# Performance work log

Measured on AMD Instinct MI355X. Metric: run time of the kernel, lower is better.

## Reference

```python
import jax, jax.numpy as jnp
import numpy as np

def setup_inputs() -> dict:
    key = jax.random.key(0)
    ks = jax.random.split(key, 7)
    T, B, I, H = 512, 128, 512, 512
    s = 1.0 / np.sqrt(H)
    return {
        "input": jax.random.normal(ks[0], (T, B, I), dtype=jnp.float32),
        "h0": jax.random.normal(ks[1], (B, H), dtype=jnp.float32),
        "c0": jax.random.normal(ks[2], (B, H), dtype=jnp.float32),
        "W_ih": jax.random.normal(ks[3], (4 * H, I), dtype=jnp.float32) * s,
        "W_hh": jax.random.normal(ks[4], (4 * H, H), dtype=jnp.float32) * s,
        "b_ih": jax.random.normal(ks[5], (4 * H,), dtype=jnp.float32) * s,
        "b_hh": jax.random.normal(ks[6], (4 * H,), dtype=jnp.float32) * s,
    }

def reference(input, h0, c0, W_ih, W_hh, b_ih, b_hh):
    H = h0.shape[-1]
    # Precompute input contribution for all timesteps: [T, B, 4H]
    x_gates = jnp.einsum('tbi,gi->tbg', input, W_ih) + b_ih + b_hh

    def step(carry, xg):
        h, c = carry
        gates = xg + h @ W_hh.T  # [B, 4H]
        i, f, g, o = jnp.split(gates, 4, axis=-1)
        i = jax.nn.sigmoid(i)
        f = jax.nn.sigmoid(f)
        g = jnp.tanh(g)
        o = jax.nn.sigmoid(o)
        c = f * c + i * g
        h = o * jnp.tanh(c)
        return (h, c), h

    (hT, cT), outputs = jax.lax.scan(step, (h0, c0), x_gates)
    return outputs, (hT, cT)
```

## Files before the change

kernel.cpp:

```cpp
#include <hip/hip_runtime.h>
#include <hip/hip_bf16.h>

#define T_STEPS 512
#define BATCH   128
#define IN      512
#define HID     512
#define KTOT    1024
#define BT      16
#define JT      32
#define NBT     8
#define NJT     16
#define BH      (BATCH * HID)

typedef __attribute__((ext_vector_type(8))) short bf16x8;
typedef __attribute__((ext_vector_type(4))) float f32x4;
typedef __attribute__((ext_vector_type(4))) unsigned int u32x4;

static __device__ __forceinline__ unsigned short f2bf(float f) {
    unsigned u = __float_as_uint(f);
    unsigned r = (u + 0x7FFFu + ((u >> 16) & 1u)) >> 16;
    return (unsigned short)r;
}
static __device__ __forceinline__ ushort4 pack4(float4 v) {
    ushort4 b4;
    b4.x = f2bf(v.x); b4.y = f2bf(v.y); b4.z = f2bf(v.z); b4.w = f2bf(v.w);
    return b4;
}
static __device__ __forceinline__ float tanh_fast(float x) {
    return 1.f - 2.f * __builtin_amdgcn_rcpf(1.f + __expf(2.f * x));
}
static __device__ __forceinline__ bool vld4(u32x4 v, unsigned tgtw) {
    return ((v[0] & 0xFFFF0000u) == tgtw) & ((v[1] & 0xFFFF0000u) == tgtw) &
           ((v[2] & 0xFFFF0000u) == tgtw) & ((v[3] & 0xFFFF0000u) == tgtw);
}

__global__ void prep_kernel(const float* __restrict__ W_ih, const float* __restrict__ W_hh,
                            const float* __restrict__ b_ih, const float* __restrict__ b_hh,
                            unsigned short* __restrict__ Wc, float* __restrict__ bias) {
    int idx = blockIdx.x * blockDim.x + threadIdx.x;
    int row = idx >> 8;
    int kq  = idx & 255;
    const float* src = (kq < 128) ? (W_ih + (size_t)row * IN + kq * 4)
                                  : (W_hh + (size_t)row * HID + (kq - 128) * 4);
    float4 v = *(const float4*)src;
    *(ushort4*)(Wc + (size_t)row * KTOT + kq * 4) = pack4(v);
    if (idx < 4 * HID) bias[idx] = b_ih[idx] + b_hh[idx];
}

__global__ __launch_bounds__(512, 2) void lstm_kernel(
    const float* __restrict__ xin, const float* __restrict__ h0,
    const float* __restrict__ c0, const unsigned short* __restrict__ Wc,
    const float* __restrict__ bias, float* __restrict__ out,
    unsigned* __restrict__ hseq)
{
    const int tid  = threadIdx.x;
    const int bid  = blockIdx.x;
    const int bt   = bid & 7;
    const int jt   = bid >> 3;
    const int wv   = tid >> 6;
    const int lane = tid & 63;
    const int ln15 = lane & 15;
    const int khi  = lane >> 4;

    __shared__ __align__(16) unsigned char smem[49152];

    const int gown = ln15 & 3;
    const int jj   = ln15 >> 2;
    const int jcol = jt * JT + wv * 4 + jj;
    const int wrow_idx = gown * HID + jcol;

    bf16x8 wfrag[32];
    {
        const unsigned short* wrow = Wc + (size_t)wrow_idx * KTOT;
        #pragma unroll
        for (int kk = 0; kk < 32; ++kk)
            wfrag[kk] = *(const bf16x8*)(wrow + kk * 32 + khi * 8);
    }
    const float biasv = bias[wrow_idx];

    float creg[4];
    #pragma unroll
    for (int R = 0; R < 4; ++R)
        creg[R] = c0[(size_t)(bt * BT + khi * 4 + R) * HID + jcol];

    const unsigned swz = (unsigned)((ln15 & 7) << 4);
    const int xrow0 = tid >> 7;
    const int xcol4 = tid & 127;

    const int q     = wv * 4 + khi;
    const int prow  = q >> 1;
    const int qh    = q & 1;
    const unsigned rsw = (unsigned)((prow & 7) << 4);

    #pragma unroll
    for (int i = 0; i < 4; ++i) {
        int row = xrow0 + 4 * i;
        unsigned off = ((unsigned)(xcol4 * 8)) ^ ((unsigned)((row & 7) << 4));
        float4 vx = *(const float4*)(xin + (size_t)(bt * BT + row) * IN + xcol4 * 4);
        *(ushort4*)(smem + (size_t)row * 1024 + off) = pack4(vx);
        float4 vh = *(const float4*)(h0 + (size_t)(bt * BT + row) * HID + xcol4 * 4);
        *(ushort4*)(smem + 16384 + (size_t)row * 1024 + off) = pack4(vh);
    }
    float4 xr[4];
    #pragma unroll
    for (int i = 0; i < 4; ++i)
        xr[i] = *(const float4*)(xin + (size_t)1 * (BATCH * IN)
                                     + (size_t)(bt * BT + xrow0 + 4 * i) * IN + xcol4 * 4);
    __syncthreads();

    f32x4 acc_x0 = {biasv, biasv, biasv, biasv};
    f32x4 acc_x1 = {0.f, 0.f, 0.f, 0.f};
    {
        const unsigned char* xrow_p = smem + (size_t)ln15 * 1024;
        #pragma unroll
        for (int kk = 0; kk < 16; ++kk) {
            unsigned off = ((unsigned)(kk * 64 + khi * 16)) ^ swz;
            bf16x8 af = *(const bf16x8*)(xrow_p + off);
            if (kk & 1) acc_x1 = __builtin_amdgcn_mfma_f32_16x16x32_bf16(af, wfrag[kk], acc_x1, 0, 0, 0);
            else        acc_x0 = __builtin_amdgcn_mfma_f32_16x16x32_bf16(af, wfrag[kk], acc_x0, 0, 0, 0);
        }
    }
    __syncthreads();

    #pragma unroll 1
    for (int t = 0; t < T_STEPS; ++t) {
        const unsigned hbase = 16384u + (unsigned)(t & 1) * 16384u;
        f32x4 acc0 = acc_x0;
        f32x4 acc1 = acc_x1;
        const unsigned char* hrow_p = smem + hbase + (size_t)ln15 * 1024;
        #pragma unroll
        for (int kk = 16; kk < 32; ++kk) {
            unsigned off = ((unsigned)((kk - 16) * 64 + khi * 16)) ^ swz;
            bf16x8 af = *(const bf16x8*)(hrow_p + off);
            if (kk & 1) acc1 = __builtin_amdgcn_mfma_f32_16x16x32_bf16(af, wfrag[kk], acc1, 0, 0, 0);
            else        acc0 = __builtin_amdgcn_mfma_f32_16x16x32_bf16(af, wfrag[kk], acc0, 0, 0, 0);
        }
        f32x4 accs = acc0 + acc1;

        float hR[4];
        const int srcbase = lane & 0x3C;
        #pragma unroll
        for (int R = 0; R < 4; ++R) {
            float x = accs[R];
            bool isg = (gown == 2);
            float e = __expf(isg ? 2.f * x : -x);
            float r = __builtin_amdgcn_rcpf(1.f + e);
            float a = isg ? 1.f - 2.f * r : r;
            float vi = __shfl(a, srcbase + 0);
            float vf = __shfl(a, srcbase + 1);
            float vg = __shfl(a, srcbase + 2);
            float vo = __shfl(a, srcbase + 3);
            float c = vf * creg[R] + vi * vg;
            creg[R] = c;
            hR[R] = vo * tanh_fast(c);
        }

        if (t == T_STEPS - 1) {
            #pragma unroll
            for (int R = 0; R < 4; ++R) {
                if (gown == R) {
                    size_t o2 = (size_t)(bt * BT + khi * 4 + R) * HID + jcol;
                    out[(size_t)t * BH + o2] = hR[R];
                    size_t base = (size_t)T_STEPS * BH;
                    out[base + o2] = hR[R];
                    out[base + BH + o2] = creg[R];
                }
            }
        } else {
            #pragma unroll
            for (int R = 0; R < 4; ++R) {
                if (gown == R) {
                    unsigned w = ((unsigned)(t + 1) << 16) | (unsigned)f2bf(hR[R]);
                    unsigned* hp = hseq + (size_t)(t & 1) * BH
                                        + (size_t)(bt * BT + khi * 4 + R) * HID + jcol;
                    asm volatile("global_store_dword %0, %1, off sc0 sc1"
                                 :: "v"(hp), "v"(w) : "memory");
                }
            }
            #pragma unroll
            for (int R = 0; R < 4; ++R) {
                if (gown == R)
                    out[(size_t)t * BH + (size_t)(bt * BT + khi * 4 + R) * HID + jcol] = hR[R];
            }

            #pragma unroll
            for (int i = 0; i < 4; ++i) {
                int row = xrow0 + 4 * i;
                unsigned off = ((unsigned)(xcol4 * 8)) ^ ((unsigned)((row & 7) << 4));
                *(ushort4*)(smem + (size_t)row * 1024 + off) = pack4(xr[i]);
            }

            asm volatile("s_waitcnt lgkmcnt(0)" ::: "memory");
            __builtin_amdgcn_s_barrier();

            const unsigned* pp = hseq + (size_t)(t & 1) * BH
                                      + (size_t)(bt * BT + prow) * HID + qh * 256 + ln15 * 4;
            const unsigned tgtw = (unsigned)(t + 1) << 16;
            u32x4 hv0, hv1, hv2, hv3;
            asm volatile(
                "global_load_dwordx4 %0, %4, off offset:0 sc0 sc1\n\t"
                "global_load_dwordx4 %1, %4, off offset:256 sc0 sc1\n\t"
                "global_load_dwordx4 %2, %4, off offset:512 sc0 sc1\n\t"
                "global_load_dwordx4 %3, %4, off offset:768 sc0 sc1"
                : "=&v"(hv0), "=&v"(hv1), "=&v"(hv2), "=&v"(hv3)
                : "v"(pp) : "memory");

            {
                int tn = (t + 2) & (T_STEPS - 1);
                #pragma unroll
                for (int i = 0; i < 4; ++i)
                    xr[i] = *(const float4*)(xin + (size_t)tn * (BATCH * IN)
                                                 + (size_t)(bt * BT + xrow0 + 4 * i) * IN + xcol4 * 4);
            }

            acc_x0 = f32x4{biasv, biasv, biasv, biasv};
            acc_x1 = f32x4{0.f, 0.f, 0.f, 0.f};
            {
                const unsigned char* xrow_p = smem + (size_t)ln15 * 1024;
                #pragma unroll
                for (int kk = 0; kk < 16; ++kk) {
                    unsigned off = ((unsigned)(kk * 64 + khi * 16)) ^ swz;
                    bf16x8 af = *(const bf16x8*)(xrow_p + off);
                    if (kk & 1) acc_x1 = __builtin_amdgcn_mfma_f32_16x16x32_bf16(af, wfrag[kk], acc_x1, 0, 0, 0);
                    else        acc_x0 = __builtin_amdgcn_mfma_f32_16x16x32_bf16(af, wfrag[kk], acc_x0, 0, 0, 0);
                }
            }

            asm volatile("s_waitcnt vmcnt(4)" ::: "memory");
            __builtin_amdgcn_sched_barrier(0);
            for (;;) {
                bool ok = vld4(hv0, tgtw) & vld4(hv1, tgtw) & vld4(hv2, tgtw) & vld4(hv3, tgtw);
                if (__ballot(ok) == ~0ull) break;
                asm volatile(
                    "global_load_dwordx4 %0, %4, off offset:0 sc0 sc1\n\t"
                    "global_load_dwordx4 %1, %4, off offset:256 sc0 sc1\n\t"
                    "global_load_dwordx4 %2, %4, off offset:512 sc0 sc1\n\t"
                    "global_load_dwordx4 %3, %4, off offset:768 sc0 sc1\n\t"
                    "s_waitcnt vmcnt(0)"
                    : "=&v"(hv0), "=&v"(hv1), "=&v"(hv2), "=&v"(hv3)
                    : "v"(pp) : "memory");
                __builtin_amdgcn_sched_barrier(0);
            }

            {
                unsigned hnb = 16384u + (unsigned)((t + 1) & 1) * 16384u;
                unsigned wbase = hnb + (unsigned)prow * 1024u;
                const u32x4 hv[4] = {hv0, hv1, hv2, hv3};
                #pragma unroll
                for (int sq = 0; sq < 4; ++sq) {
                    uint2 pk;
                    pk.x = (hv[sq][0] & 0xFFFFu) | (hv[sq][1] << 16);
                    pk.y = (hv[sq][2] & 0xFFFFu) | (hv[sq][3] << 16);
                    unsigned off = ((unsigned)(qh * 512 + sq * 128 + ln15 * 8)) ^ rsw;
                    *(uint2*)(smem + wbase + off) = pk;
                }
            }

            asm volatile("s_waitcnt lgkmcnt(0)" ::: "memory");
            __builtin_amdgcn_s_barrier();
        }
    }
}

extern "C" void kernel_launch(void* const* d_in, const int* in_sizes, int n_in,
                              void* d_out, int out_size, void* d_ws, size_t ws_size,
                              hipStream_t stream) {
    const float* input = (const float*)d_in[0];
    const float* h0    = (const float*)d_in[1];
    const float* c0    = (const float*)d_in[2];
    const float* W_ih  = (const float*)d_in[3];
    const float* W_hh  = (const float*)d_in[4];
    const float* b_ih  = (const float*)d_in[5];
    const float* b_hh  = (const float*)d_in[6];
    float* out = (float*)d_out;

    char* ws = (char*)d_ws;
    unsigned* hseq = (unsigned*)ws;
    float*    bias = (float*)(ws + 512 * 1024);
    unsigned short* Wc = (unsigned short*)(ws + 512 * 1024 + 16 * 1024);

    hipMemsetAsync(hseq, 0, 2 * BH * sizeof(unsigned), stream);
    prep_kernel<<<2048, 256, 0, stream>>>(W_ih, W_hh, b_ih, b_hh, Wc, bias);
    lstm_kernel<<<NBT * NJT, 512, 0, stream>>>(input, h0, c0, Wc, bias, out, hseq);
}
```

Measured before the change: 1.917 ms.

## Process two batch tiles per block, halving grid, and use DPP quad broadcast

```diff
diff --git a/kernel.cpp b/kernel.cpp
--- a/kernel.cpp
+++ b/kernel.cpp
@@ -8,7 +8,6 @@
 #define KTOT    1024
 #define BT      16
 #define JT      32
-#define NBT     8
 #define NJT     16
 #define BH      (BATCH * HID)
 
@@ -32,6 +31,11 @@
 static __device__ __forceinline__ bool vld4(u32x4 v, unsigned tgtw) {
     return ((v[0] & 0xFFFF0000u) == tgtw) & ((v[1] & 0xFFFF0000u) == tgtw) &
            ((v[2] & 0xFFFF0000u) == tgtw) & ((v[3] & 0xFFFF0000u) == tgtw);
+}
+template<int I>
+static __device__ __forceinline__ float qbcast(float x) {
+    return __uint_as_float((unsigned)__builtin_amdgcn_update_dpp(
+        (int)__float_as_uint(x), (int)__float_as_uint(x), I * 0x55, 0xF, 0xF, false));
 }
 
 __global__ void prep_kernel(const float* __restrict__ W_ih, const float* __restrict__ W_hh,
@@ -55,14 +59,16 @@
 {
     const int tid  = threadIdx.x;
     const int bid  = blockIdx.x;
-    const int bt   = bid & 7;
-    const int jt   = bid >> 3;
+    const int gp   = bid & 3;
+    const int jt   = bid >> 2;
+    const int btA  = gp * 2;
+    const int btB  = gp * 2 + 1;
     const int wv   = tid >> 6;
     const int lane = tid & 63;
     const int ln15 = lane & 15;
     const int khi  = lane >> 4;
 
-    __shared__ __align__(16) unsigned char smem[49152];
+    __shared__ __align__(16) unsigned char smem[98304];
 
     const int gown = ln15 & 3;
     const int jj   = ln15 >> 2;
@@ -78,10 +84,12 @@
     }
     const float biasv = bias[wrow_idx];
 
-    float creg[4];
+    float cregA[4], cregB[4];
     #pragma unroll
-    for (int R = 0; R < 4; ++R)
-        creg[R] = c0[(size_t)(bt * BT + khi * 4 + R) * HID + jcol];
+    for (int R = 0; R < 4; ++R) {
+        cregA[R] = c0[(size_t)(btA * BT + khi * 4 + R) * HID + jcol];
+        cregB[R] = c0[(size_t)(btB * BT + khi * 4 + R) * HID + jcol];
+    }
 
     const unsigned swz = (unsigned)((ln15 & 7) << 4);
     const int xrow0 = tid >> 7;
@@ -96,163 +104,239 @@
     for (int i = 0; i < 4; ++i) {
         int row = xrow0 + 4 * i;
         unsigned off = ((unsigned)(xcol4 * 8)) ^ ((unsigned)((row & 7) << 4));
-        float4 vx = *(const float4*)(xin + (size_t)(bt * BT + row) * IN + xcol4 * 4);
-        *(ushort4*)(smem + (size_t)row * 1024 + off) = pack4(vx);
-        float4 vh = *(const float4*)(h0 + (size_t)(bt * BT + row) * HID + xcol4 * 4);
-        *(ushort4*)(smem + 16384 + (size_t)row * 1024 + off) = pack4(vh);
-    }
-    float4 xr[4];
+        float4 vA = *(const float4*)(xin + (size_t)(btA * BT + row) * IN + xcol4 * 4);
+        *(ushort4*)(smem + (size_t)row * 1024 + off) = pack4(vA);
+        float4 vB = *(const float4*)(xin + (size_t)(btB * BT + row) * IN + xcol4 * 4);
+        *(ushort4*)(smem + 16384 + (size_t)row * 1024 + off) = pack4(vB);
+        float4 hA = *(const float4*)(h0 + (size_t)(btA * BT + row) * HID + xcol4 * 4);
+        *(ushort4*)(smem + 32768 + (size_t)row * 1024 + off) = pack4(hA);
+        float4 hB = *(const float4*)(h0 + (size_t)(btB * BT + row) * HID + xcol4 * 4);
+        *(ushort4*)(smem + 65536 + (size_t)row * 1024 + off) = pack4(hB);
+    }
+    float4 xrA[4], xrB[4];
     #pragma unroll
-    for (int i = 0; i < 4; ++i)
-        xr[i] = *(const float4*)(xin + (size_t)1 * (BATCH * IN)
-                                     + (size_t)(bt * BT + xrow0 + 4 * i) * IN + xcol4 * 4);
+    for (int i = 0; i < 4; ++i) {
+        xrA[i] = *(const float4*)(xin + (size_t)1 * (BATCH * IN)
+                                      + (size_t)(btA * BT + xrow0 + 4 * i) * IN + xcol4 * 4);
+        xrB[i] = *(const float4*)(xin + (size_t)1 * (BATCH * IN)
+                                      + (size_t)(btB * BT + xrow0 + 4 * i) * IN + xcol4 * 4);
+    }
     __syncthreads();
 
-    f32x4 acc_x0 = {biasv, biasv, biasv, biasv};
-    f32x4 acc_x1 = {0.f, 0.f, 0.f, 0.f};
+    f32x4 acc_xA0 = {biasv, biasv, biasv, biasv}, acc_xA1 = {0.f, 0.f, 0.f, 0.f};
+    f32x4 acc_xB0 = {biasv, biasv, biasv, biasv}, acc_xB1 = {0.f, 0.f, 0.f, 0.f};
     {
-        const unsigned char* xrow_p = smem + (size_t)ln15 * 1024;
+        const unsigned char* xa = smem + (size_t)ln15 * 1024;
+        const unsigned char* xb = smem + 16384 + (size_t)ln15 * 1024;
         #pragma unroll
         for (int kk = 0; kk < 16; ++kk) {
             unsigned off = ((unsigned)(kk * 64 + khi * 16)) ^ swz;
-            bf16x8 af = *(const bf16x8*)(xrow_p + off);
-            if (kk & 1) acc_x1 = __builtin_amdgcn_mfma_f32_16x16x32_bf16(af, wfrag[kk], acc_x1, 0, 0, 0);
-            else        acc_x0 = __builtin_amdgcn_mfma_f32_16x16x32_bf16(af, wfrag[kk], acc_x0, 0, 0, 0);
+            bf16x8 afA = *(const bf16x8*)(xa + off);
+            bf16x8 afB = *(const bf16x8*)(xb + off);
+            if (kk & 1) { acc_xA1 = __builtin_amdgcn_mfma_f32_16x16x32_bf16(afA, wfrag[kk], acc_xA1, 0, 0, 0);
+                          acc_xB1 = __builtin_amdgcn_mfma_f32_16x16x32_bf16(afB, wfrag[kk], acc_xB1, 0, 0, 0); }
+            else        { acc_xA0 = __builtin_amdgcn_mfma_f32_16x16x32_bf16(afA, wfrag[kk], acc_xA0, 0, 0, 0);
+                          acc_xB0 = __builtin_amdgcn_mfma_f32_16x16x32_bf16(afB, wfrag[kk], acc_xB0, 0, 0, 0); }
         }
     }
     __syncthreads();
 
     #pragma unroll 1
     for (int t = 0; t < T_STEPS; ++t) {
-        const unsigned hbase = 16384u + (unsigned)(t & 1) * 16384u;
-        f32x4 acc0 = acc_x0;
-        f32x4 acc1 = acc_x1;
-        const unsigned char* hrow_p = smem + hbase + (size_t)ln15 * 1024;
-        #pragma unroll
-        for (int kk = 16; kk < 32; ++kk) {
-            unsigned off = ((unsigned)((kk - 16) * 64 + khi * 16)) ^ swz;
-            bf16x8 af = *(const bf16x8*)(hrow_p + off);
-            if (kk & 1) acc1 = __builtin_amdgcn_mfma_f32_16x16x32_bf16(af, wfrag[kk], acc1, 0, 0, 0);
-            else        acc0 = __builtin_amdgcn_mfma_f32_16x16x32_bf16(af, wfrag[kk], acc0, 0, 0, 0);
+        const unsigned hsA = 32768u + (unsigned)(t & 1) * 16384u;
+        const unsigned hsB = 65536u + (unsigned)(t & 1) * 16384u;
+        float hRA[4], hRB[4];
+
+        {
+            f32x4 a0 = acc_xA0, a1 = acc_xA1;
+            const unsigned char* hp = smem + hsA + (size_t)ln15 * 1024;
+            #pragma unroll
+            for (int kk = 16; kk < 32; ++kk) {
+                unsigned off = ((unsigned)((kk - 16) * 64 + khi * 16)) ^ swz;
+                bf16x8 af = *(const bf16x8*)(hp + off);
+                if (kk & 1) a1 = __builtin_amdgcn_mfma_f32_16x16x32_bf16(af, wfrag[kk], a1, 0, 0, 0);
+                else        a0 = __builtin_amdgcn_mfma_f32_16x16x32_bf16(af, wfrag[kk], a0, 0, 0, 0);
+            }
+            f32x4 accs = a0 + a1;
+            #pragma unroll
+            for (int R = 0; R < 4; ++R) {
+                float x = accs[R];
+                bool isg = (gown == 2);
+                float e = __expf(isg ? 2.f * x : -x);
+                float r = __builtin_amdgcn_rcpf(1.f + e);
+                float a = isg ? 1.f - 2.f * r : r;
+                float vi = qbcast<0>(a), vf = qbcast<1>(a), vg = qbcast<2>(a), vo = qbcast<3>(a);
+                float c = vf * cregA[R] + vi * vg;
+                cregA[R] = c;
+                hRA[R] = vo * tanh_fast(c);
+            }
+            if (t < T_STEPS - 1) {
+                #pragma unroll
+                for (int R = 0; R < 4; ++R) {
+                    if (gown == R) {
+                        unsigned w = ((unsigned)(t + 1) << 16) | (unsigned)f2bf(hRA[R]);
+                        unsigned* hq = hseq + (size_t)(t & 1) * BH
+                                            + (size_t)(btA * BT + khi * 4 + R) * HID + jcol;
+                        asm volatile("global_store_dword %0, %1, off sc0 sc1" :: "v"(hq), "v"(w) : "memory");
+                    }
+                }
+            }
+            #pragma unroll
+            for (int R = 0; R < 4; ++R) {
+                if (gown == R)
+                    out[(size_t)t * BH + (size_t)(btA * BT + khi * 4 + R) * HID + jcol] = hRA[R];
+            }
         }
-        f32x4 accs = acc0 + acc1;
-
-        float hR[4];
-        const int srcbase = lane & 0x3C;
-        #pragma unroll
-        for (int R = 0; R < 4; ++R) {
-            float x = accs[R];
-            bool isg = (gown == 2);
-            float e = __expf(isg ? 2.f * x : -x);
-            float r = __builtin_amdgcn_rcpf(1.f + e);
-            float a = isg ? 1.f - 2.f * r : r;
-            float vi = __shfl(a, srcbase + 0);
-            float vf = __shfl(a, srcbase + 1);
-            float vg = __shfl(a, srcbase + 2);
-            float vo = __shfl(a, srcbase + 3);
-            float c = vf * creg[R] + vi * vg;
-            creg[R] = c;
-            hR[R] = vo * tanh_fast(c);
+
+        {
+            f32x4 a0 = acc_xB0, a1 = acc_xB1;
+            const unsigned char* hp = smem + hsB + (size_t)ln15 * 1024;
+            #pragma unroll
+            for (int kk = 16; kk < 32; ++kk) {
+                unsigned off = ((unsigned)((kk - 16) * 64 + khi * 16)) ^ swz;
+                bf16x8 af = *(const bf16x8*)(hp + off);
+                if (kk & 1) a1 = __builtin_amdgcn_mfma_f32_16x16x32_bf16(af, wfrag[kk], a1, 0, 0, 0);
+                else        a0 = __builtin_amdgcn_mfma_f32_16x16x32_bf16(af, wfrag[kk], a0, 0, 0, 0);
+            }
+            f32x4 accs = a0 + a1;
+            #pragma unroll
+            for (int R = 0; R < 4; ++R) {
+                float x = accs[R];
+                bool isg = (gown == 2);
+                float e = __expf(isg ? 2.f * x : -x);
+                float r = __builtin_amdgcn_rcpf(1.f + e);
+                float a = isg ? 1.f - 2.f * r : r;
+                float vi = qbcast<0>(a), vf = qbcast<1>(a), vg = qbcast<2>(a), vo = qbcast<3>(a);
+                float c = vf * cregB[R] + vi * vg;
+                cregB[R] = c;
+                hRB[R] = vo * tanh_fast(c);
+            }
+            if (t < T_STEPS - 1) {
+                #pragma unroll
+                for (int R = 0; R < 4; ++R) {
+                    if (gown == R) {
+                        unsigned w = ((unsigned)(t + 1) << 16) | (unsigned)f2bf(hRB[R]);
+                        unsigned* hq = hseq + (size_t)(t & 1) * BH
+                                            + (size_t)(btB * BT + khi * 4 + R) * HID + jcol;
+                        asm volatile("global_store_dword %0, %1, off sc0 sc1" :: "v"(hq), "v"(w) : "memory");
+                    }
+                }
+            }
+            #pragma unroll
+            for (int R = 0; R < 4; ++R) {
+                if (gown == R)
+                    out[(size_t)t * BH + (size_t)(btB * BT + khi * 4 + R) * HID + jcol] = hRB[R];
+            }
         }
 
         if (t == T_STEPS - 1) {
+            size_t base = (size_t)T_STEPS * BH;
             #pragma unroll
             for (int R = 0; R < 4; ++R) {
                 if (gown == R) {
-                    size_t o2 = (size_t)(bt * BT + khi * 4 + R) * HID + jcol;
-                    out[(size_t)t * BH + o2] = hR[R];
-                    size_t base = (size_t)T_STEPS * BH;
-                    out[base + o2] = hR[R];
-                    out[base + BH + o2] = creg[R];
+                    size_t oA = (size_t)(btA * BT + khi * 4 + R) * HID + jcol;
+                    out[base + oA] = hRA[R];
+                    out[base + BH + oA] = cregA[R];
+                    size_t oB = (size_t)(btB * BT + khi * 4 + R) * HID + jcol;
+                    out[base + oB] = hRB[R];
+                    out[base + BH + oB] = cregB[R];
                 }
             }
         } else {
-            #pragma unroll
-            for (int R = 0; R < 4; ++R) {
-                if (gown == R) {
-                    unsigned w = ((unsigned)(t + 1) << 16) | (unsigned)f2bf(hR[R]);
-                    unsigned* hp = hseq + (size_t)(t & 1) * BH
-                                        + (size_t)(bt * BT + khi * 4 + R) * HID + jcol;
-                    asm volatile("global_store_dword %0, %1, off sc0 sc1"
-                                 :: "v"(hp), "v"(w) : "memory");
-                }
-            }
-            #pragma unroll
-            for (int R = 0; R < 4; ++R) {
-                if (gown == R)
-                    out[(size_t)t * BH + (size_t)(bt * BT + khi * 4 + R) * HID + jcol] = hR[R];
-            }
-
             #pragma unroll
             for (int i = 0; i < 4; ++i) {
                 int row = xrow0 + 4 * i;
                 unsigned off = ((unsigned)(xcol4 * 8)) ^ ((unsigned)((row & 7) << 4));
-                *(ushort4*)(smem + (size_t)row * 1024 + off) = pack4(xr[i]);
-            }
-
+                *(ushort4*)(smem + (size_t)row * 1024 + off) = pack4(xrA[i]);
+                *(ushort4*)(smem + 16384 + (size_t)row * 1024 + off) = pack4(xrB[i]);
+            }
             asm volatile("s_waitcnt lgkmcnt(0)" ::: "memory");
             __builtin_amdgcn_s_barrier();
 
-            const unsigned* pp = hseq + (size_t)(t & 1) * BH
-                                      + (size_t)(bt * BT + prow) * HID + qh * 256 + ln15 * 4;
+            const unsigned* ppA = hseq + (size_t)(t & 1) * BH
+                                       + (size_t)(btA * BT + prow) * HID + qh * 256 + ln15 * 4;
+            const unsigned* ppB = hseq + (size_t)(t & 1) * BH
+                                       + (size_t)(btB * BT + prow) * HID + qh * 256 + ln15 * 4;
             const unsigned tgtw = (unsigned)(t + 1) << 16;
-            u32x4 hv0, hv1, hv2, hv3;
+            u32x4 hA0, hA1, hA2, hA3, hB0, hB1, hB2, hB3;
             asm volatile(
-                "global_load_dwordx4 %0, %4, off offset:0 sc0 sc1\n\t"
-                "global_load_dwordx4 %1, %4, off offset:256 sc0 sc1\n\t"
-                "global_load_dwordx4 %2, %4, off offset:512 sc0 sc1\n\t"
-                "global_load_dwordx4 %3, %4, off offset:768 sc0 sc1"
-                : "=&v"(hv0), "=&v"(hv1), "=&v"(hv2), "=&v"(hv3)
-                : "v"(pp) : "memory");
+                "global_load_dwordx4 %0, %8, off offset:0 sc0 sc1\n\t"
+                "global_load_dwordx4 %1, %8, off offset:256 sc0 sc1\n\t"
+                "global_load_dwordx4 %2, %8, off offset:512 sc0 sc1\n\t"
+                "global_load_dwordx4 %3, %8, off offset:768 sc0 sc1\n\t"
+                "global_load_dwordx4 %4, %9, off offset:0 sc0 sc1\n\t"
+                "global_load_dwordx4 %5, %9, off offset:256 sc0 sc1\n\t"
+                "global_load_dwordx4 %6, %9, off offset:512 sc0 sc1\n\t"
+                "global_load_dwordx4 %7, %9, off offset:768 sc0 sc1"
+                : "=&v"(hA0), "=&v"(hA1), "=&v"(hA2), "=&v"(hA3),
+                  "=&v"(hB0), "=&v"(hB1), "=&v"(hB2), "=&v"(hB3)
+                : "v"(ppA), "v"(ppB) : "memory");
 
             {
                 int tn = (t + 2) & (T_STEPS - 1);
                 #pragma unroll
-                for (int i = 0; i < 4; ++i)
-                    xr[i] = *(const float4*)(xin + (size_t)tn * (BATCH * IN)
-                                                 + (size_t)(bt * BT + xrow0 + 4 * i) * IN + xcol4 * 4);
-            }
-
-            acc_x0 = f32x4{biasv, biasv, biasv, biasv};
-            acc_x1 = f32x4{0.f, 0.f, 0.f, 0.f};
+                for (int i = 0; i < 4; ++i) {
+                    xrA[i] = *(const float4*)(xin + (size_t)tn * (BATCH * IN)
+                                                  + (size_t)(btA * BT + xrow0 + 4 * i) * IN + xcol4 * 4);
+                    xrB[i] = *(const float4*)(xin + (size_t)tn * (BATCH * IN)
+                                                  + (size_t)(btB * BT + xrow0 + 4 * i) * IN + xcol4 * 4);
+                }
+            }
+
+            acc_xA0 = f32x4{biasv, biasv, biasv, biasv}; acc_xA1 = f32x4{0.f, 0.f, 0.f, 0.f};
+            acc_xB0 = f32x4{biasv, biasv, biasv, biasv}; acc_xB1 = f32x4{0.f, 0.f, 0.f, 0.f};
             {
-                const unsigned char* xrow_p = smem + (size_t)ln15 * 1024;
+                const unsigned char* xa = smem + (size_t)ln15 * 1024;
+                const unsigned char* xb = smem + 16384 + (size_t)ln15 * 1024;
                 #pragma unroll
                 for (int kk = 0; kk < 16; ++kk) {
                     unsigned off = ((unsigned)(kk * 64 + khi * 16)) ^ swz;
-                    bf16x8 af = *(const bf16x8*)(xrow_p + off);
-                    if (kk & 1) acc_x1 = __builtin_amdgcn_mfma_f32_16x16x32_bf16(af, wfrag[kk], acc_x1, 0, 0, 0);
-                    else        acc_x0 = __builtin_amdgcn_mfma_f32_16x16x32_bf16(af, wfrag[kk], acc_x0, 0, 0, 0);
-                }
-            }
-
-            asm volatile("s_waitcnt vmcnt(4)" ::: "memory");
+                    bf16x8 afA = *(const bf16x8*)(xa + off);
+                    bf16x8 afB = *(const bf16x8*)(xb + off);
+                    if (kk & 1) { acc_xA1 = __builtin_amdgcn_mfma_f32_16x16x32_bf16(afA, wfrag[kk], acc_xA1, 0, 0, 0);
+                                  acc_xB1 = __builtin_amdgcn_mfma_f32_16x16x32_bf16(afB, wfrag[kk], acc_xB1, 0, 0, 0); }
+                    else        { acc_xA0 = __builtin_amdgcn_mfma_f32_16x16x32_bf16(afA, wfrag[kk], acc_xA0, 0, 0, 0);
+                                  acc_xB0 = __builtin_amdgcn_mfma_f32_16x16x32_bf16(afB, wfrag[kk], acc_xB0, 0, 0, 0); }
+                }
+            }
+
+            asm volatile("s_waitcnt vmcnt(8)" ::: "memory");
             __builtin_amdgcn_sched_barrier(0);
             for (;;) {
-                bool ok = vld4(hv0, tgtw) & vld4(hv1, tgtw) & vld4(hv2, tgtw) & vld4(hv3, tgtw);
+                bool ok = vld4(hA0, tgtw) & vld4(hA1, tgtw) & vld4(hA2, tgtw) & vld4(hA3, tgtw)
+                        & vld4(hB0, tgtw) & vld4(hB1, tgtw) & vld4(hB2, tgtw) & vld4(hB3, tgtw);
                 if (__ballot(ok) == ~0ull) break;
                 asm volatile(
-                    "global_load_dwordx4 %0, %4, off offset:0 sc0 sc1\n\t"
-                    "global_load_dwordx4 %1, %4, off offset:256 sc0 sc1\n\t"
-                    "global_load_dwordx4 %2, %4, off offset:512 sc0 sc1\n\t"
-                    "global_load_dwordx4 %3, %4, off offset:768 sc0 sc1\n\t"
+                    "global_load_dwordx4 %0, %8, off offset:0 sc0 sc1\n\t"
+                    "global_load_dwordx4 %1, %8, off offset:256 sc0 sc1\n\t"
+                    "global_load_dwordx4 %2, %8, off offset:512 sc0 sc1\n\t"
+                    "global_load_dwordx4 %3, %8, off offset:768 sc0 sc1\n\t"
+                    "global_load_dwordx4 %4, %9, off offset:0 sc0 sc1\n\t"
+                    "global_load_dwordx4 %5, %9, off offset:256 sc0 sc1\n\t"
+                    "global_load_dwordx4 %6, %9, off offset:512 sc0 sc1\n\t"
+                    "global_load_dwordx4 %7, %9, off offset:768 sc0 sc1\n\t"
                     "s_waitcnt vmcnt(0)"
-                    : "=&v"(hv0), "=&v"(hv1), "=&v"(hv2), "=&v"(hv3)
-                    : "v"(pp) : "memory");
+                    : "=&v"(hA0), "=&v"(hA1), "=&v"(hA2), "=&v"(hA3),
+                      "=&v"(hB0), "=&v"(hB1), "=&v"(hB2), "=&v"(hB3)
+                    : "v"(ppA), "v"(ppB) : "memory");
                 __builtin_amdgcn_sched_barrier(0);
             }
 
             {
-                unsigned hnb = 16384u + (unsigned)((t + 1) & 1) * 16384u;
-                unsigned wbase = hnb + (unsigned)prow * 1024u;
-                const u32x4 hv[4] = {hv0, hv1, hv2, hv3};
+                unsigned wbA = 32768u + (unsigned)((t + 1) & 1) * 16384u + (unsigned)prow * 1024u;
+                unsigned wbB = 65536u + (unsigned)((t + 1) & 1) * 16384u + (unsigned)prow * 1024u;
+                const u32x4 hvA[4] = {hA0, hA1, hA2, hA3};
+                const u32x4 hvB[4] = {hB0, hB1, hB2, hB3};
                 #pragma unroll
                 for (int sq = 0; sq < 4; ++sq) {
-                    uint2 pk;
-                    pk.x = (hv[sq][0] & 0xFFFFu) | (hv[sq][1] << 16);
-                    pk.y = (hv[sq][2] & 0xFFFFu) | (hv[sq][3] << 16);
                     unsigned off = ((unsigned)(qh * 512 + sq * 128 + ln15 * 8)) ^ rsw;
-                    *(uint2*)(smem + wbase + off) = pk;
+                    uint2 pkA, pkB;
+                    pkA.x = (hvA[sq][0] & 0xFFFFu) | (hvA[sq][1] << 16);
+                    pkA.y = (hvA[sq][2] & 0xFFFFu) | (hvA[sq][3] << 16);
+                    pkB.x = (hvB[sq][0] & 0xFFFFu) | (hvB[sq][1] << 16);
+                    pkB.y = (hvB[sq][2] & 0xFFFFu) | (hvB[sq][3] << 16);
+                    *(uint2*)(smem + wbA + off) = pkA;
+                    *(uint2*)(smem + wbB + off) = pkB;
                 }
             }
 
@@ -281,5 +365,5 @@
 
     hipMemsetAsync(hseq, 0, 2 * BH * sizeof(unsigned), stream);
     prep_kernel<<<2048, 256, 0, stream>>>(W_ih, W_hh, b_ih, b_hh, Wc, bias);
-    lstm_kernel<<<NBT * NJT, 512, 0, stream>>>(input, h0, c0, Wc, bias, out, hseq);
-}
+    lstm_kernel<<<NJT * 4, 512, 0, stream>>>(input, h0, c0, Wc, bias, out, hseq);
+}
```

Result: slower. 6.830 ms (+256.3%).

## Issue second speculative h poll mid-MFMA, use DPP broadcast, store h earlier

Applied to the files above, without the earlier changes.

```diff
diff --git a/kernel.cpp b/kernel.cpp
--- a/kernel.cpp
+++ b/kernel.cpp
@@ -32,6 +32,11 @@
 static __device__ __forceinline__ bool vld4(u32x4 v, unsigned tgtw) {
     return ((v[0] & 0xFFFF0000u) == tgtw) & ((v[1] & 0xFFFF0000u) == tgtw) &
            ((v[2] & 0xFFFF0000u) == tgtw) & ((v[3] & 0xFFFF0000u) == tgtw);
+}
+template<int I>
+static __device__ __forceinline__ float qbcast(float x) {
+    return __uint_as_float((unsigned)__builtin_amdgcn_update_dpp(
+        (int)__float_as_uint(x), (int)__float_as_uint(x), I * 0x55, 0xF, 0xF, false));
 }
 
 __global__ void prep_kernel(const float* __restrict__ W_ih, const float* __restrict__ W_hh,
@@ -138,7 +143,6 @@
         f32x4 accs = acc0 + acc1;
 
         float hR[4];
-        const int srcbase = lane & 0x3C;
         #pragma unroll
         for (int R = 0; R < 4; ++R) {
             float x = accs[R];
@@ -146,43 +150,33 @@
             float e = __expf(isg ? 2.f * x : -x);
             float r = __builtin_amdgcn_rcpf(1.f + e);
             float a = isg ? 1.f - 2.f * r : r;
-            float vi = __shfl(a, srcbase + 0);
-            float vf = __shfl(a, srcbase + 1);
-            float vg = __shfl(a, srcbase + 2);
-            float vo = __shfl(a, srcbase + 3);
+            float vi = qbcast<0>(a), vf = qbcast<1>(a), vg = qbcast<2>(a), vo = qbcast<3>(a);
             float c = vf * creg[R] + vi * vg;
             creg[R] = c;
-            hR[R] = vo * tanh_fast(c);
+            float h = vo * tanh_fast(c);
+            hR[R] = h;
+            if (t < T_STEPS - 1 && gown == R) {
+                unsigned w = ((unsigned)(t + 1) << 16) | (unsigned)f2bf(h);
+                unsigned* hp = hseq + (size_t)(t & 1) * BH
+                                    + (size_t)(bt * BT + khi * 4 + R) * HID + jcol;
+                asm volatile("global_store_dword %0, %1, off sc0 sc1"
+                             :: "v"(hp), "v"(w) : "memory");
+            }
+            if (gown == R)
+                out[(size_t)t * BH + (size_t)(bt * BT + khi * 4 + R) * HID + jcol] = h;
         }
 
         if (t == T_STEPS - 1) {
+            size_t base = (size_t)T_STEPS * BH;
             #pragma unroll
             for (int R = 0; R < 4; ++R) {
                 if (gown == R) {
                     size_t o2 = (size_t)(bt * BT + khi * 4 + R) * HID + jcol;
-                    out[(size_t)t * BH + o2] = hR[R];
-                    size_t base = (size_t)T_STEPS * BH;
                     out[base + o2] = hR[R];
                     out[base + BH + o2] = creg[R];
                 }
             }
         } else {
-            #pragma unroll
-            for (int R = 0; R < 4; ++R) {
-                if (gown == R) {
-                    unsigned w = ((unsigned)(t + 1) << 16) | (unsigned)f2bf(hR[R]);
-                    unsigned* hp = hseq + (size_t)(t & 1) * BH
-                                        + (size_t)(bt * BT + khi * 4 + R) * HID + jcol;
-                    asm volatile("global_store_dword %0, %1, off sc0 sc1"
-                                 :: "v"(hp), "v"(w) : "memory");
-                }
-            }
-            #pragma unroll
-            for (int R = 0; R < 4; ++R) {
-                if (gown == R)
-                    out[(size_t)t * BH + (size_t)(bt * BT + khi * 4 + R) * HID + jcol] = hR[R];
-            }
-
             #pragma unroll
             for (int i = 0; i < 4; ++i) {
                 int row = xrow0 + 4 * i;
@@ -205,6 +199,34 @@
                 : "=&v"(hv0), "=&v"(hv1), "=&v"(hv2), "=&v"(hv3)
                 : "v"(pp) : "memory");
 
+            acc_x0 = f32x4{biasv, biasv, biasv, biasv};
+            acc_x1 = f32x4{0.f, 0.f, 0.f, 0.f};
+            const unsigned char* xrow_p = smem + (size_t)ln15 * 1024;
+            #pragma unroll
+            for (int kk = 0; kk < 8; ++kk) {
+                unsigned off = ((unsigned)(kk * 64 + khi * 16)) ^ swz;
+                bf16x8 af = *(const bf16x8*)(xrow_p + off);
+                if (kk & 1) acc_x1 = __builtin_amdgcn_mfma_f32_16x16x32_bf16(af, wfrag[kk], acc_x1, 0, 0, 0);
+                else        acc_x0 = __builtin_amdgcn_mfma_f32_16x16x32_bf16(af, wfrag[kk], acc_x0, 0, 0, 0);
+            }
+
+            u32x4 hw0, hw1, hw2, hw3;
+            asm volatile(
+                "global_load_dwordx4 %0, %4, off offset:0 sc0 sc1\n\t"
+                "global_load_dwordx4 %1, %4, off offset:256 sc0 sc1\n\t"
+                "global_load_dwordx4 %2, %4, off offset:512 sc0 sc1\n\t"
+                "global_load_dwordx4 %3, %4, off offset:768 sc0 sc1"
+                : "=&v"(hw0), "=&v"(hw1), "=&v"(hw2), "=&v"(hw3)
+                : "v"(pp) : "memory");
+
+            #pragma unroll
+            for (int kk = 8; kk < 16; ++kk) {
+                unsigned off = ((unsigned)(kk * 64 + khi * 16)) ^ swz;
+                bf16x8 af = *(const bf16x8*)(xrow_p + off);
+                if (kk & 1) acc_x1 = __builtin_amdgcn_mfma_f32_16x16x32_bf16(af, wfrag[kk], acc_x1, 0, 0, 0);
+                else        acc_x0 = __builtin_amdgcn_mfma_f32_16x16x32_bf16(af, wfrag[kk], acc_x0, 0, 0, 0);
+            }
+
             {
                 int tn = (t + 2) & (T_STEPS - 1);
                 #pragma unroll
@@ -213,33 +235,32 @@
                                                  + (size_t)(bt * BT + xrow0 + 4 * i) * IN + xcol4 * 4);
             }
 
-            acc_x0 = f32x4{biasv, biasv, biasv, biasv};
-            acc_x1 = f32x4{0.f, 0.f, 0.f, 0.f};
-            {
-                const unsigned char* xrow_p = smem + (size_t)ln15 * 1024;
-                #pragma unroll
-                for (int kk = 0; kk < 16; ++kk) {
-                    unsigned off = ((unsigned)(kk * 64 + khi * 16)) ^ swz;
-                    bf16x8 af = *(const bf16x8*)(xrow_p + off);
-                    if (kk & 1) acc_x1 = __builtin_amdgcn_mfma_f32_16x16x32_bf16(af, wfrag[kk], acc_x1, 0, 0, 0);
-                    else        acc_x0 = __builtin_amdgcn_mfma_f32_16x16x32_bf16(af, wfrag[kk], acc_x0, 0, 0, 0);
+            asm volatile("s_waitcnt vmcnt(8)" ::: "memory");
+            __builtin_amdgcn_sched_barrier(0);
+            bool ok0 = vld4(hv0, tgtw) & vld4(hv1, tgtw) & vld4(hv2, tgtw) & vld4(hv3, tgtw);
+            if (__ballot(ok0) == ~0ull) {
+                asm volatile("s_waitcnt vmcnt(4)" ::: "memory");
+            } else {
+                asm volatile("s_waitcnt vmcnt(4)" ::: "memory");
+                __builtin_amdgcn_sched_barrier(0);
+                bool ok1 = vld4(hw0, tgtw) & vld4(hw1, tgtw) & vld4(hw2, tgtw) & vld4(hw3, tgtw);
+                if (__ballot(ok1) == ~0ull) {
+                    hv0 = hw0; hv1 = hw1; hv2 = hw2; hv3 = hw3;
+                } else {
+                    for (;;) {
+                        asm volatile(
+                            "global_load_dwordx4 %0, %4, off offset:0 sc0 sc1\n\t"
+                            "global_load_dwordx4 %1, %4, off offset:256 sc0 sc1\n\t"
+                            "global_load_dwordx4 %2, %4, off offset:512 sc0 sc1\n\t"
+                            "global_load_dwordx4 %3, %4, off offset:768 sc0 sc1\n\t"
+                            "s_waitcnt vmcnt(0)"
+                            : "=&v"(hv0), "=&v"(hv1), "=&v"(hv2), "=&v"(hv3)
+                            : "v"(pp) : "memory");
+                        __builtin_amdgcn_sched_barrier(0);
+                        bool ok = vld4(hv0, tgtw) & vld4(hv1, tgtw) & vld4(hv2, tgtw) & vld4(hv3, tgtw);
+                        if (__ballot(ok) == ~0ull) break;
+                    }
                 }
-            }
-
-            asm volatile("s_waitcnt vmcnt(4)" ::: "memory");
-            __builtin_amdgcn_sched_barrier(0);
-            for (;;) {
-                bool ok = vld4(hv0, tgtw) & vld4(hv1, tgtw) & vld4(hv2, tgtw) & vld4(hv3, tgtw);
-                if (__ballot(ok) == ~0ull) break;
-                asm volatile(
-                    "global_load_dwordx4 %0, %4, off offset:0 sc0 sc1\n\t"
-                    "global_load_dwordx4 %1, %4, off offset:256 sc0 sc1\n\t"
-                    "global_load_dwordx4 %2, %4, off offset:512 sc0 sc1\n\t"
-                    "global_load_dwordx4 %3, %4, off offset:768 sc0 sc1\n\t"
-                    "s_waitcnt vmcnt(0)"
-                    : "=&v"(hv0), "=&v"(hv1), "=&v"(hv2), "=&v"(hv3)
-                    : "v"(pp) : "memory");
-                __builtin_amdgcn_sched_barrier(0);
             }
 
             {
```

After: 1.867 ms. 1.03x faster.
